# Kernel tuning notes

Hardware: AMD Instinct MI355X
Metric: run time of the kernel (lower is better)

## Reference

```python
import jax, jax.numpy as jnp
import numpy as np


def setup_inputs() -> dict:
    key = jax.random.key(0)
    ks = jax.random.split(key, 5)
    B, C, H, W = 16, 512, 64, 64
    cm = cn = C // 4  # int(C*0.5*0.5)
    # kaiming_normal fan_out for 1x1 conv: std = sqrt(2 / out_channels)
    def kaiming(k, out_c, in_c):
        return jax.random.normal(k, (out_c, in_c), jnp.float32) * np.sqrt(2.0 / out_c)
    return {
        "x": jax.random.normal(ks[0], (B, C, H, W), jnp.float32),
        "WA": kaiming(ks[1], cm, C), "bA": jnp.zeros((cm,), jnp.float32),
        "WB": kaiming(ks[2], cn, C), "bB": jnp.zeros((cn,), jnp.float32),
        "WV": kaiming(ks[3], cn, C), "bV": jnp.zeros((cn,), jnp.float32),
        "WR": kaiming(ks[4], C, cm), "bR": jnp.zeros((C,), jnp.float32),
    }


def reference(x, WA, bA, WB, bB, WV, bV, WR, bR):
    b, c, h, w = x.shape
    n = h * w
    xf = x.reshape(b, c, n)  # [b, c, n] flattened spatial
    # 1x1 convs == per-pixel GEMMs
    A = jnp.einsum('mc,bcn->bmn', WA, xf) + bA[None, :, None]          # [b, cm, n]
    Bm = jax.nn.softmax(jnp.einsum('mc,bcn->bmn', WB, xf) + bB[None, :, None], axis=1)  # softmax over channels
    Vm = jax.nn.softmax(jnp.einsum('mc,bcn->bmn', WV, xf) + bV[None, :, None], axis=1)
    # second-order pooling: global descriptors [b, cm, cn]
    gd = jnp.einsum('bmn,bkn->bmk', A, Bm)
    # distribute: [b, cm, n]
    Z = jnp.einsum('bmk,bkn->bmn', gd, Vm)
    # reconstruct 1x1 conv back to c channels
    out = jnp.einsum('cm,bmn->bcn', WR, Z) + bR[None, :, None]
    return out.reshape(b, c, h, w)
```

## Files before the change

kernel.cpp:

```cpp
#include <hip/hip_runtime.h>
#include <hip/hip_fp16.h>


typedef _Float16 half8 __attribute__((ext_vector_type(8)));
typedef float f32x4 __attribute__((ext_vector_type(4)));

__device__ __forceinline__ unsigned short f2h(float v) {
  return __builtin_bit_cast(unsigned short, (_Float16)v);
}

__device__ __forceinline__ f32x4 mfma16(half8 a, half8 b, f32x4 c) {
  return __builtin_amdgcn_mfma_f32_16x16x32_f16(a, b, c, 0, 0, 0);
}

__device__ __forceinline__ void stage_tile(unsigned short* lds,
                                           const unsigned short* g,
                                           int gs, int k0) {
  const int tid = threadIdx.x;
#pragma unroll
  for (int i = 0; i < 2; ++i) {
    int c = tid + 256 * i;
    int row = c >> 2, q = c & 3;
    uint4 v = *(const uint4*)&g[(size_t)row * gs + k0 + q * 8];
    int kgA = (q & 1) * 2, h = q >> 1;
    *(uint2*)&lds[(kgA * 128 + row) * 8 + h * 4]       = make_uint2(v.x, v.y);
    *(uint2*)&lds[((kgA + 1) * 128 + row) * 8 + h * 4] = make_uint2(v.z, v.w);
  }
}

__device__ __forceinline__ half8 ld_frag(const unsigned short* lds, int row) {
  int kg = (threadIdx.x & 63) >> 4;
  uint4 u = *(const uint4*)&lds[(kg * 128 + row) * 8];
  return __builtin_bit_cast(half8, u);
}

__global__ __launch_bounds__(256) void k_prep_w(
    const float* __restrict__ WA, const float* __restrict__ WB,
    const float* __restrict__ WV, const float* __restrict__ WR,
    unsigned short* __restrict__ Wh, unsigned short* __restrict__ WRh) {
  int idx = blockIdx.x * 256 + threadIdx.x;
  if (idx < 196608) {
    int mg = idx >> 16, r = idx & 65535;
    const float* src = (mg == 0) ? WA : ((mg == 1) ? WB : WV);
    Wh[idx] = f2h(src[r]);
  } else {
    int r = idx - 196608;
    WRh[r] = f2h(WR[r]);
  }
}

__global__ __launch_bounds__(256) void k_transpose_x(
    const float* __restrict__ x, unsigned short* __restrict__ xT) {
  const int n0 = blockIdx.x * 32, c0 = blockIdx.y * 32, b = blockIdx.z;
  __shared__ unsigned short sT[32][33];
  const int t = threadIdx.x;
  {
    int cr = t >> 3, nc = (t & 7) * 4;
    float4 v = *(const float4*)&x[((size_t)b * 512 + c0 + cr) * 4096 + n0 + nc];
    sT[cr][nc + 0] = f2h(v.x);
    sT[cr][nc + 1] = f2h(v.y);
    sT[cr][nc + 2] = f2h(v.z);
    sT[cr][nc + 3] = f2h(v.w);
  }
  __syncthreads();
  {
    int nr = t >> 3, cc = (t & 7) * 4;
    ushort4 o;
    o.x = sT[cc + 0][nr]; o.y = sT[cc + 1][nr];
    o.z = sT[cc + 2][nr]; o.w = sT[cc + 3][nr];
    *(ushort4*)&xT[((size_t)b * 4096 + n0 + nr) * 512 + c0 + cc] = o;
  }
}

__global__ __launch_bounds__(256) void k_gemm_abv(
    const unsigned short* __restrict__ xT, const unsigned short* __restrict__ Wh,
    const float* __restrict__ bA, const float* __restrict__ bB,
    const float* __restrict__ bV,
    unsigned short* __restrict__ Aout, unsigned short* __restrict__ Bmout,
    unsigned short* __restrict__ VmTout) {
  const int nt = blockIdx.x, mg = blockIdx.y, b = blockIdx.z;
  const int tid = threadIdx.x, lane = tid & 63;
  const int w = tid >> 6, wr = w >> 1, wc = w & 1;
  const int kg = lane >> 4, lidx = lane & 15;

  __shared__ unsigned short sW[4096], sX[4096];
  __shared__ float colmax[2][128], colsum[2][128], sBias[128];

  const float* bias = (mg == 0) ? bA : ((mg == 1) ? bB : bV);
  if (tid < 128) sBias[tid] = bias[tid];

  const unsigned short* Wg = Wh + (size_t)mg * 128 * 512;
  const unsigned short* Xg = xT + ((size_t)b * 4096 + (size_t)nt * 128) * 512;

  f32x4 acc[4][4];
#pragma unroll
  for (int mf = 0; mf < 4; ++mf)
#pragma unroll
    for (int nf = 0; nf < 4; ++nf) acc[mf][nf] = (f32x4){0.f, 0.f, 0.f, 0.f};

  for (int k0 = 0; k0 < 512; k0 += 32) {
    stage_tile(sW, Wg, 512, k0);
    stage_tile(sX, Xg, 512, k0);
    __syncthreads();
    half8 af[4];
#pragma unroll
    for (int mf = 0; mf < 4; ++mf) af[mf] = ld_frag(sW, wr * 64 + mf * 16 + lidx);
#pragma unroll
    for (int nf = 0; nf < 4; ++nf) {
      half8 bf = ld_frag(sX, wc * 64 + nf * 16 + lidx);
#pragma unroll
      for (int mf = 0; mf < 4; ++mf) acc[mf][nf] = mfma16(af[mf], bf, acc[mf][nf]);
    }
    __syncthreads();
  }

#pragma unroll
  for (int mf = 0; mf < 4; ++mf)
#pragma unroll
    for (int i = 0; i < 4; ++i) {
      float bb = sBias[wr * 64 + mf * 16 + kg * 4 + i];
#pragma unroll
      for (int nf = 0; nf < 4; ++nf) acc[mf][nf][i] += bb;
    }

  const size_t bofs = (size_t)b * 128 * 4096;
  if (mg == 0) {
#pragma unroll
    for (int mf = 0; mf < 4; ++mf)
#pragma unroll
      for (int nf = 0; nf < 4; ++nf)
#pragma unroll
        for (int i = 0; i < 4; ++i) {
          int m_ = wr * 64 + mf * 16 + kg * 4 + i;
          int n_ = nt * 128 + wc * 64 + nf * 16 + lidx;
          Aout[bofs + (size_t)m_ * 4096 + n_] = f2h(acc[mf][nf][i]);
        }
    return;
  }

  float cmax[4], csum[4];
#pragma unroll
  for (int nf = 0; nf < 4; ++nf) {
    float m = -1e30f;
#pragma unroll
    for (int mf = 0; mf < 4; ++mf)
#pragma unroll
      for (int i = 0; i < 4; ++i) m = fmaxf(m, acc[mf][nf][i]);
    m = fmaxf(m, __shfl_xor(m, 16));
    m = fmaxf(m, __shfl_xor(m, 32));
    cmax[nf] = m;
  }
  if (kg == 0) {
#pragma unroll
    for (int nf = 0; nf < 4; ++nf) colmax[wr][wc * 64 + nf * 16 + lidx] = cmax[nf];
  }
  __syncthreads();
#pragma unroll
  for (int nf = 0; nf < 4; ++nf)
    cmax[nf] = fmaxf(cmax[nf], colmax[wr ^ 1][wc * 64 + nf * 16 + lidx]);
#pragma unroll
  for (int nf = 0; nf < 4; ++nf) {
    float s = 0.f;
#pragma unroll
    for (int mf = 0; mf < 4; ++mf)
#pragma unroll
      for (int i = 0; i < 4; ++i) {
        float e = __expf(acc[mf][nf][i] - cmax[nf]);
        acc[mf][nf][i] = e;
        s += e;
      }
    s += __shfl_xor(s, 16);
    s += __shfl_xor(s, 32);
    csum[nf] = s;
  }
  if (kg == 0) {
#pragma unroll
    for (int nf = 0; nf < 4; ++nf) colsum[wr][wc * 64 + nf * 16 + lidx] = csum[nf];
  }
  __syncthreads();
  float inv_s[4];
#pragma unroll
  for (int nf = 0; nf < 4; ++nf)
    inv_s[nf] = 1.f / (csum[nf] + colsum[wr ^ 1][wc * 64 + nf * 16 + lidx]);

  if (mg == 1) {
#pragma unroll
    for (int mf = 0; mf < 4; ++mf)
#pragma unroll
      for (int nf = 0; nf < 4; ++nf)
#pragma unroll
        for (int i = 0; i < 4; ++i) {
          int m_ = wr * 64 + mf * 16 + kg * 4 + i;
          int n_ = nt * 128 + wc * 64 + nf * 16 + lidx;
          Bmout[bofs + (size_t)m_ * 4096 + n_] = f2h(acc[mf][nf][i] * inv_s[nf]);
        }
  } else {
    const size_t vofs = (size_t)b * 4096 * 128;
#pragma unroll
    for (int mf = 0; mf < 4; ++mf)
#pragma unroll
      for (int nf = 0; nf < 4; ++nf) {
        int m0 = wr * 64 + mf * 16 + kg * 4;
        int n_ = nt * 128 + wc * 64 + nf * 16 + lidx;
        ushort4 pk;
        pk.x = f2h(acc[mf][nf][0] * inv_s[nf]);
        pk.y = f2h(acc[mf][nf][1] * inv_s[nf]);
        pk.z = f2h(acc[mf][nf][2] * inv_s[nf]);
        pk.w = f2h(acc[mf][nf][3] * inv_s[nf]);
        *(ushort4*)&VmTout[vofs + (size_t)n_ * 128 + m0] = pk;
      }
  }
}

__global__ __launch_bounds__(256) void k_gd(
    const unsigned short* __restrict__ A, const unsigned short* __restrict__ Bm,
    float* __restrict__ gd) {
  const int ks = blockIdx.x, b = blockIdx.y;
  const int tid = threadIdx.x, lane = tid & 63;
  const int w = tid >> 6, wr = w >> 1, wc = w & 1;
  const int kg = lane >> 4, lidx = lane & 15;
  __shared__ unsigned short sA[4096], sB[4096];
  const unsigned short* Ab = A + (size_t)b * 128 * 4096 + (size_t)ks * 256;
  const unsigned short* Bb = Bm + (size_t)b * 128 * 4096 + (size_t)ks * 256;

  f32x4 acc[4][4];
#pragma unroll
  for (int mf = 0; mf < 4; ++mf)
#pragma unroll
    for (int nf = 0; nf < 4; ++nf) acc[mf][nf] = (f32x4){0.f, 0.f, 0.f, 0.f};

  for (int k0 = 0; k0 < 256; k0 += 32) {
    stage_tile(sA, Ab, 4096, k0);
    stage_tile(sB, Bb, 4096, k0);
    __syncthreads();
    half8 af[4];
#pragma unroll
    for (int mf = 0; mf < 4; ++mf) af[mf] = ld_frag(sA, wr * 64 + mf * 16 + lidx);
#pragma unroll
    for (int nf = 0; nf < 4; ++nf) {
      half8 bf = ld_frag(sB, wc * 64 + nf * 16 + lidx);
#pragma unroll
      for (int mf = 0; mf < 4; ++mf) acc[mf][nf] = mfma16(af[mf], bf, acc[mf][nf]);
    }
    __syncthreads();
  }
  float* gb = gd + (size_t)b * 128 * 128;
#pragma unroll
  for (int mf = 0; mf < 4; ++mf)
#pragma unroll
    for (int nf = 0; nf < 4; ++nf)
#pragma unroll
      for (int i = 0; i < 4; ++i) {
        int m_ = wr * 64 + mf * 16 + kg * 4 + i;
        int k2 = wc * 64 + nf * 16 + lidx;
        atomicAdd(&gb[(size_t)m_ * 128 + k2], acc[mf][nf][i]);
      }
}

__global__ __launch_bounds__(256) void k_z(
    const float* __restrict__ gd, const unsigned short* __restrict__ VmT,
    unsigned short* __restrict__ ZT) {
  const int nt = blockIdx.x, b = blockIdx.y;
  const int tid = threadIdx.x, lane = tid & 63;
  const int w = tid >> 6, wr = w >> 1, wc = w & 1;
  const int kg = lane >> 4, lidx = lane & 15;
  __shared__ unsigned short sG[4096], sV[4096];
  const float4* gb = (const float4*)(gd + (size_t)b * 128 * 128);
  const unsigned short* Vb = VmT + ((size_t)b * 4096 + (size_t)nt * 128) * 128;

  f32x4 acc[4][4];
#pragma unroll
  for (int mf = 0; mf < 4; ++mf)
#pragma unroll
    for (int nf = 0; nf < 4; ++nf) acc[mf][nf] = (f32x4){0.f, 0.f, 0.f, 0.f};

  for (int k0 = 0; k0 < 128; k0 += 32) {
#pragma unroll
    for (int i = 0; i < 4; ++i) {
      int c = tid + 256 * i;
      int row = c >> 3, q8 = c & 7;
      float4 v = gb[row * 32 + (k0 >> 2) + q8];
      unsigned int lo = (unsigned)f2h(v.x) | ((unsigned)f2h(v.y) << 16);
      unsigned int hi = (unsigned)f2h(v.z) | ((unsigned)f2h(v.w) << 16);
      int kgq = q8 & 3, h = q8 >> 2;
      *(uint2*)&sG[(kgq * 128 + row) * 8 + h * 4] = make_uint2(lo, hi);
    }
    stage_tile(sV, Vb, 128, k0);
    __syncthreads();
    half8 af[4];
#pragma unroll
    for (int mf = 0; mf < 4; ++mf) af[mf] = ld_frag(sG, wr * 64 + mf * 16 + lidx);
#pragma unroll
    for (int nf = 0; nf < 4; ++nf) {
      half8 bf = ld_frag(sV, wc * 64 + nf * 16 + lidx);
#pragma unroll
      for (int mf = 0; mf < 4; ++mf) acc[mf][nf] = mfma16(af[mf], bf, acc[mf][nf]);
    }
    __syncthreads();
  }
  const size_t zofs = (size_t)b * 4096 * 128;
#pragma unroll
  for (int mf = 0; mf < 4; ++mf)
#pragma unroll
    for (int nf = 0; nf < 4; ++nf) {
      int m0 = wr * 64 + mf * 16 + kg * 4;
      int n_ = nt * 128 + wc * 64 + nf * 16 + lidx;
      ushort4 pk;
      pk.x = f2h(acc[mf][nf][0]);
      pk.y = f2h(acc[mf][nf][1]);
      pk.z = f2h(acc[mf][nf][2]);
      pk.w = f2h(acc[mf][nf][3]);
      *(ushort4*)&ZT[zofs + (size_t)n_ * 128 + m0] = pk;
    }
}

__global__ __launch_bounds__(256) void k_out(
    const unsigned short* __restrict__ WRh, const unsigned short* __restrict__ ZT,
    const float* __restrict__ bR, float* __restrict__ out) {
  const int nt = blockIdx.x, ct = blockIdx.y, b = blockIdx.z;
  const int tid = threadIdx.x, lane = tid & 63;
  const int w = tid >> 6, wr = w >> 1, wc = w & 1;
  const int kg = lane >> 4, lidx = lane & 15;
  __shared__ unsigned short sW[4096], sZ[4096];
  __shared__ float sBias[128];
  if (tid < 128) sBias[tid] = bR[ct * 128 + tid];
  const unsigned short* Wb = WRh + (size_t)ct * 128 * 128;
  const unsigned short* Zb = ZT + ((size_t)b * 4096 + (size_t)nt * 128) * 128;

  f32x4 acc[4][4];
#pragma unroll
  for (int mf = 0; mf < 4; ++mf)
#pragma unroll
    for (int nf = 0; nf < 4; ++nf) acc[mf][nf] = (f32x4){0.f, 0.f, 0.f, 0.f};

  for (int k0 = 0; k0 < 128; k0 += 32) {
    stage_tile(sW, Wb, 128, k0);
    stage_tile(sZ, Zb, 128, k0);
    __syncthreads();
    half8 af[4];
#pragma unroll
    for (int mf = 0; mf < 4; ++mf) af[mf] = ld_frag(sW, wr * 64 + mf * 16 + lidx);
#pragma unroll
    for (int nf = 0; nf < 4; ++nf) {
      half8 bf = ld_frag(sZ, wc * 64 + nf * 16 + lidx);
#pragma unroll
      for (int mf = 0; mf < 4; ++mf) acc[mf][nf] = mfma16(af[mf], bf, acc[mf][nf]);
    }
    __syncthreads();
  }
#pragma unroll
  for (int mf = 0; mf < 4; ++mf)
#pragma unroll
    for (int nf = 0; nf < 4; ++nf)
#pragma unroll
      for (int i = 0; i < 4; ++i) {
        int cl = wr * 64 + mf * 16 + kg * 4 + i;
        int n_ = nt * 128 + wc * 64 + nf * 16 + lidx;
        out[((size_t)b * 512 + ct * 128 + cl) * 4096 + n_] = acc[mf][nf][i] + sBias[cl];
      }
}

extern "C" void kernel_launch(void* const* d_in, const int* in_sizes, int n_in,
                              void* d_out, int out_size, void* d_ws, size_t ws_size,
                              hipStream_t stream) {
  const float* x  = (const float*)d_in[0];
  const float* WA = (const float*)d_in[1];
  const float* bA = (const float*)d_in[2];
  const float* WB = (const float*)d_in[3];
  const float* bB = (const float*)d_in[4];
  const float* WV = (const float*)d_in[5];
  const float* bV = (const float*)d_in[6];
  const float* WR = (const float*)d_in[7];
  const float* bR = (const float*)d_in[8];
  float* out = (float*)d_out;

  char* ws = (char*)d_ws;
  unsigned short* Wh   = (unsigned short*)(ws);
  unsigned short* WRh  = (unsigned short*)(ws + 393216);
  unsigned short* xT   = (unsigned short*)(ws + 524288);
  unsigned short* Aout = (unsigned short*)(ws + 67633152);
  unsigned short* Bm   = (unsigned short*)(ws + 84410368);
  unsigned short* VmT  = (unsigned short*)(ws + 101187584);
  float*          gd   = (float*)(ws + 117964800);
  unsigned short* ZT   = (unsigned short*)(ws + 119013376);

  hipMemsetAsync(gd, 0, (size_t)16 * 128 * 128 * sizeof(float), stream);
  k_prep_w<<<1024, 256, 0, stream>>>(WA, WB, WV, WR, Wh, WRh);
  k_transpose_x<<<dim3(128, 16, 16), 256, 0, stream>>>(x, xT);
  k_gemm_abv<<<dim3(32, 3, 16), 256, 0, stream>>>(xT, Wh, bA, bB, bV, Aout, Bm, VmT);
  k_gd<<<dim3(16, 16), 256, 0, stream>>>(Aout, Bm, gd);
  k_z<<<dim3(32, 16), 256, 0, stream>>>(gd, VmT, ZT);
  k_out<<<dim3(32, 4, 16), 256, 0, stream>>>(WRh, ZT, bR, out);
}
```

Baseline: 172.9 us.

## Use direct global-to-LDS loads with pre-permuted K layouts across GEMM stages

Replaces the register-staged LDS tile fill with `global_load_lds` 16-byte direct copies in all four GEMM kernels. To make a plain linear copy land in the fragment-friendly LDS layout, every producer (weight prep, x transpose, A/Bm/VmT/ZT epilogues) now writes its K dimension permuted within 32-element groups. The x transpose also moves to 64x64 fp32 tiles, converting to fp16 on the way out. This removes VGPR round-trips and LDS store instructions in the main loops. The cost is a coupled layout contract between kernels, which breaks if any producer misses the permutation.

```diff
diff --git a/kernel.cpp b/kernel.cpp
--- a/kernel.cpp
+++ b/kernel.cpp
@@ -13,18 +13,27 @@
   return __builtin_amdgcn_mfma_f32_16x16x32_f16(a, b, c, 0, 0, 0);
 }
 
-__device__ __forceinline__ void stage_tile(unsigned short* lds,
+__device__ __forceinline__ int perm32(int v) {
+  return (((v & 15) >> 2) << 3) | (((v >> 4) & 1) << 2) | (v & 3);
+}
+
+__device__ __forceinline__ void glds16(const unsigned short* g, unsigned short* l) {
+  __builtin_amdgcn_global_load_lds(
+      (const __attribute__((address_space(1))) unsigned int*)g,
+      (__attribute__((address_space(3))) unsigned int*)l, 16, 0, 0);
+}
+
+__device__ __forceinline__ void stage_glds(unsigned short* lds,
                                            const unsigned short* g,
                                            int gs, int k0) {
-  const int tid = threadIdx.x;
-#pragma unroll
-  for (int i = 0; i < 2; ++i) {
-    int c = tid + 256 * i;
-    int row = c >> 2, q = c & 3;
-    uint4 v = *(const uint4*)&g[(size_t)row * gs + k0 + q * 8];
-    int kgA = (q & 1) * 2, h = q >> 1;
-    *(uint2*)&lds[(kgA * 128 + row) * 8 + h * 4]       = make_uint2(v.x, v.y);
-    *(uint2*)&lds[((kgA + 1) * 128 + row) * 8 + h * 4] = make_uint2(v.z, v.w);
+  const int lane = threadIdx.x & 63;
+  const int w = threadIdx.x >> 6;
+#pragma unroll
+  for (int p = 0; p < 2; ++p) {
+    int g0 = (w + p * 4) * 64;
+    int gi = g0 + lane;
+    int row = gi & 127, kg = gi >> 7;
+    glds16(g + (size_t)row * gs + k0 + kg * 8, lds + g0 * 8);
   }
 }
 
@@ -42,33 +51,36 @@
   if (idx < 196608) {
     int mg = idx >> 16, r = idx & 65535;
     const float* src = (mg == 0) ? WA : ((mg == 1) ? WB : WV);
-    Wh[idx] = f2h(src[r]);
+    Wh[(idx & ~31) | perm32(idx & 31)] = f2h(src[r]);
   } else {
     int r = idx - 196608;
-    WRh[r] = f2h(WR[r]);
+    WRh[(r & ~31) | perm32(r & 31)] = f2h(WR[r]);
   }
 }
 
 __global__ __launch_bounds__(256) void k_transpose_x(
     const float* __restrict__ x, unsigned short* __restrict__ xT) {
-  const int n0 = blockIdx.x * 32, c0 = blockIdx.y * 32, b = blockIdx.z;
-  __shared__ unsigned short sT[32][33];
+  const int n0 = blockIdx.x * 64, c0 = blockIdx.y * 64, b = blockIdx.z;
+  __shared__ float sT[64][65];
   const int t = threadIdx.x;
-  {
-    int cr = t >> 3, nc = (t & 7) * 4;
-    float4 v = *(const float4*)&x[((size_t)b * 512 + c0 + cr) * 4096 + n0 + nc];
-    sT[cr][nc + 0] = f2h(v.x);
-    sT[cr][nc + 1] = f2h(v.y);
-    sT[cr][nc + 2] = f2h(v.z);
-    sT[cr][nc + 3] = f2h(v.w);
+  const int tr = t >> 4, tc4 = (t & 15) * 4;
+#pragma unroll
+  for (int i = 0; i < 4; ++i) {
+    int c = tr + i * 16;
+    float4 v = *(const float4*)&x[((size_t)b * 512 + c0 + c) * 4096 + n0 + tc4];
+    sT[c][tc4 + 0] = v.x; sT[c][tc4 + 1] = v.y;
+    sT[c][tc4 + 2] = v.z; sT[c][tc4 + 3] = v.w;
   }
   __syncthreads();
-  {
-    int nr = t >> 3, cc = (t & 7) * 4;
+#pragma unroll
+  for (int i = 0; i < 4; ++i) {
+    int n = tr + i * 16;
+    int cq = tc4;
     ushort4 o;
-    o.x = sT[cc + 0][nr]; o.y = sT[cc + 1][nr];
-    o.z = sT[cc + 2][nr]; o.w = sT[cc + 3][nr];
-    *(ushort4*)&xT[((size_t)b * 4096 + n0 + nr) * 512 + c0 + cc] = o;
+    o.x = f2h(sT[cq + 0][n]); o.y = f2h(sT[cq + 1][n]);
+    o.z = f2h(sT[cq + 2][n]); o.w = f2h(sT[cq + 3][n]);
+    int cperm = c0 + (cq & ~31) + perm32(cq & 31);
+    *(ushort4*)&xT[((size_t)b * 4096 + n0 + n) * 512 + cperm] = o;
   }
 }
 
@@ -99,8 +111,8 @@
     for (int nf = 0; nf < 4; ++nf) acc[mf][nf] = (f32x4){0.f, 0.f, 0.f, 0.f};
 
   for (int k0 = 0; k0 < 512; k0 += 32) {
-    stage_tile(sW, Wg, 512, k0);
-    stage_tile(sX, Xg, 512, k0);
+    stage_glds(sW, Wg, 512, k0);
+    stage_glds(sX, Xg, 512, k0);
     __syncthreads();
     half8 af[4];
 #pragma unroll
@@ -123,6 +135,13 @@
       for (int nf = 0; nf < 4; ++nf) acc[mf][nf][i] += bb;
     }
 
+  int npg[4];
+#pragma unroll
+  for (int nf = 0; nf < 4; ++nf) {
+    int nin = nf * 16 + lidx;
+    npg[nf] = nt * 128 + wc * 64 + (nin & ~31) + perm32(nin & 31);
+  }
+
   const size_t bofs = (size_t)b * 128 * 4096;
   if (mg == 0) {
 #pragma unroll
@@ -132,8 +151,7 @@
 #pragma unroll
         for (int i = 0; i < 4; ++i) {
           int m_ = wr * 64 + mf * 16 + kg * 4 + i;
-          int n_ = nt * 128 + wc * 64 + nf * 16 + lidx;
-          Aout[bofs + (size_t)m_ * 4096 + n_] = f2h(acc[mf][nf][i]);
+          Aout[bofs + (size_t)m_ * 4096 + npg[nf]] = f2h(acc[mf][nf][i]);
         }
     return;
   }
@@ -191,8 +209,7 @@
 #pragma unroll
         for (int i = 0; i < 4; ++i) {
           int m_ = wr * 64 + mf * 16 + kg * 4 + i;
-          int n_ = nt * 128 + wc * 64 + nf * 16 + lidx;
-          Bmout[bofs + (size_t)m_ * 4096 + n_] = f2h(acc[mf][nf][i] * inv_s[nf]);
+          Bmout[bofs + (size_t)m_ * 4096 + npg[nf]] = f2h(acc[mf][nf][i] * inv_s[nf]);
         }
   } else {
     const size_t vofs = (size_t)b * 4096 * 128;
@@ -201,13 +218,14 @@
 #pragma unroll
       for (int nf = 0; nf < 4; ++nf) {
         int m0 = wr * 64 + mf * 16 + kg * 4;
+        int mp = (m0 & ~31) + perm32(m0 & 31);
         int n_ = nt * 128 + wc * 64 + nf * 16 + lidx;
         ushort4 pk;
         pk.x = f2h(acc[mf][nf][0] * inv_s[nf]);
         pk.y = f2h(acc[mf][nf][1] * inv_s[nf]);
         pk.z = f2h(acc[mf][nf][2] * inv_s[nf]);
         pk.w = f2h(acc[mf][nf][3] * inv_s[nf]);
-        *(ushort4*)&VmTout[vofs + (size_t)n_ * 128 + m0] = pk;
+        *(ushort4*)&VmTout[vofs + (size_t)n_ * 128 + mp] = pk;
       }
   }
 }
@@ -230,8 +248,8 @@
     for (int nf = 0; nf < 4; ++nf) acc[mf][nf] = (f32x4){0.f, 0.f, 0.f, 0.f};
 
   for (int k0 = 0; k0 < 256; k0 += 32) {
-    stage_tile(sA, Ab, 4096, k0);
-    stage_tile(sB, Bb, 4096, k0);
+    stage_glds(sA, Ab, 4096, k0);
+    stage_glds(sB, Bb, 4096, k0);
     __syncthreads();
     half8 af[4];
 #pragma unroll
@@ -285,7 +303,7 @@
       int kgq = q8 & 3, h = q8 >> 2;
       *(uint2*)&sG[(kgq * 128 + row) * 8 + h * 4] = make_uint2(lo, hi);
     }
-    stage_tile(sV, Vb, 128, k0);
+    stage_glds(sV, Vb, 128, k0);
     __syncthreads();
     half8 af[4];
 #pragma unroll
@@ -304,13 +322,14 @@
 #pragma unroll
     for (int nf = 0; nf < 4; ++nf) {
       int m0 = wr * 64 + mf * 16 + kg * 4;
+      int mp = (m0 & ~31) + perm32(m0 & 31);
       int n_ = nt * 128 + wc * 64 + nf * 16 + lidx;
       ushort4 pk;
       pk.x = f2h(acc[mf][nf][0]);
       pk.y = f2h(acc[mf][nf][1]);
       pk.z = f2h(acc[mf][nf][2]);
       pk.w = f2h(acc[mf][nf][3]);
-      *(ushort4*)&ZT[zofs + (size_t)n_ * 128 + m0] = pk;
+      *(ushort4*)&ZT[zofs + (size_t)n_ * 128 + mp] = pk;
     }
 }
 
@@ -334,8 +353,8 @@
     for (int nf = 0; nf < 4; ++nf) acc[mf][nf] = (f32x4){0.f, 0.f, 0.f, 0.f};
 
   for (int k0 = 0; k0 < 128; k0 += 32) {
-    stage_tile(sW, Wb, 128, k0);
-    stage_tile(sZ, Zb, 128, k0);
+    stage_glds(sW, Wb, 128, k0);
+    stage_glds(sZ, Zb, 128, k0);
     __syncthreads();
     half8 af[4];
 #pragma unroll
@@ -386,7 +405,7 @@
 
   hipMemsetAsync(gd, 0, (size_t)16 * 128 * 128 * sizeof(float), stream);
   k_prep_w<<<1024, 256, 0, stream>>>(WA, WB, WV, WR, Wh, WRh);
-  k_transpose_x<<<dim3(128, 16, 16), 256, 0, stream>>>(x, xT);
+  k_transpose_x<<<dim3(64, 8, 16), 256, 0, stream>>>(x, xT);
   k_gemm_abv<<<dim3(32, 3, 16), 256, 0, stream>>>(xT, Wh, bA, bB, bV, Aout, Bm, VmT);
   k_gd<<<dim3(16, 16), 256, 0, stream>>>(Aout, Bm, gd);
   k_z<<<dim3(32, 16), 256, 0, stream>>>(gd, VmT, ZT);
```

After: 184.0 us (median of 5 runs). +6.4%, slower.
